# Optimization experiments

Hardware: AMD Instinct MI355X
Metric: run time of the kernel (lower is better)

## Reference

```python
import jax, jax.numpy as jnp
import numpy as np

NUM_EXPERTS = 8
TOP_K = 2
D_HIDDEN = 2048
D_EXPERT = 1024
N_TOKENS = 4096


def setup_inputs() -> dict:
    key = jax.random.key(0)
    ks = jax.random.split(key, 8)
    s_d = 1.0 / np.sqrt(D_HIDDEN).astype(np.float32)
    s_h = 1.0 / np.sqrt(D_EXPERT).astype(np.float32)
    return {
        "x": jax.random.normal(ks[0], (N_TOKENS, D_HIDDEN), jnp.float32),
        "W_g": jax.random.normal(ks[1], (D_HIDDEN, NUM_EXPERTS), jnp.float32) * s_d,
        "W_gate": jax.random.normal(ks[2], (NUM_EXPERTS, D_HIDDEN, D_EXPERT), jnp.float32) * s_d,
        "W_up": jax.random.normal(ks[3], (NUM_EXPERTS, D_HIDDEN, D_EXPERT), jnp.float32) * s_d,
        "W_down": jax.random.normal(ks[4], (NUM_EXPERTS, D_EXPERT, D_HIDDEN), jnp.float32) * s_h,
        "Ws_gate": jax.random.normal(ks[5], (D_HIDDEN, D_EXPERT), jnp.float32) * s_d,
        "Ws_up": jax.random.normal(ks[6], (D_HIDDEN, D_EXPERT), jnp.float32) * s_d,
        "Ws_down": jax.random.normal(ks[7], (D_EXPERT, D_HIDDEN), jnp.float32) * s_h,
    }


def reference(x, W_g, W_gate, W_up, W_down, Ws_gate, Ws_up, Ws_down):
    # Router: softmax logits -> top-k scores/indices (fused_gating_topk)
    probs = jax.nn.softmax(x @ W_g, axis=-1)                      # [N, E]
    scores, idx = jax.lax.top_k(probs, TOP_K)                     # [N, K]
    # Per-(token, expert) combine weight; zero for unrouted experts.
    combine = (jax.nn.one_hot(idx, NUM_EXPERTS, dtype=x.dtype) * scores[..., None]).sum(axis=1)  # [N, E]

    # Routed experts: fused gate/up SiLU with per-token weight scaling, then down-proj.
    gate = jnp.einsum('nd,edh->enh', x, W_gate)                   # [E, N, H]
    up = jnp.einsum('nd,edh->enh', x, W_up)                       # [E, N, H]
    h = jax.nn.silu(gate) * up * combine.T[:, :, None]            # weight=0 kills unrouted tokens
    out = jnp.einsum('enh,ehd->nd', h, W_down)                    # [N, D]

    # Shared expert applied to every token (no routing weight).
    shared = (jax.nn.silu(x @ Ws_gate) * (x @ Ws_up)) @ Ws_down
    return out + shared
```

## Files before the change

kernel.cpp:

```cpp
#include <hip/hip_runtime.h>
#include <cstdint>
#include <cstddef>

#define N_TOK 4096
#define D_HID 2048
#define D_EXP 1024
#define NE 8
#define N_ROUTED (N_TOK * 2)
#define N_ROWS (N_ROUTED + N_TOK)
#define MAX_BLK 56
#define NT1 (D_HID / 32)
#define NT2 (D_EXP / 32)

typedef unsigned short u16;
typedef __bf16 bf16x8 __attribute__((ext_vector_type(8)));
typedef float f32x4 __attribute__((ext_vector_type(4)));

constexpr size_t OFF_XB    = 0;
constexpr size_t OFF_WG    = OFF_XB    + 16777216;
constexpr size_t OFF_WU    = OFF_WG    + 33554432;
constexpr size_t OFF_WD    = OFF_WU    + 33554432;
constexpr size_t OFF_WSG   = OFF_WD    + 33554432;
constexpr size_t OFF_WSU   = OFF_WSG   + 4194304;
constexpr size_t OFF_WSD   = OFF_WSU   + 4194304;
constexpr size_t OFF_H     = OFF_WSD   + 4194304;
constexpr size_t OFF_ROWS  = OFF_H     + 25165824;
constexpr size_t OFF_WSLOT = OFF_ROWS  + 49152;
constexpr size_t OFF_SEG   = OFF_WSLOT + 49152;
constexpr size_t OFF_BLK   = OFF_SEG   + 128;
constexpr size_t OFF_TOPI  = OFF_BLK   + 768;
constexpr size_t OFF_TOPW  = OFF_TOPI  + 32768;
constexpr size_t OFF_INV   = OFF_TOPW  + 32768;
constexpr size_t OFF_H2    = OFF_WG;

__device__ __forceinline__ u16 f32_to_bf16(float f) {
    union { float f; unsigned int u; } c; c.f = f;
    unsigned int u = c.u;
    return (u16)((u + 0x7FFFu + ((u >> 16) & 1u)) >> 16);
}
__device__ __forceinline__ float bf16_to_f32(u16 v) {
    union { unsigned int u; float f; } c; c.u = ((unsigned int)v) << 16;
    return c.f;
}

__device__ __forceinline__ void gld_lds16(const u16* g, u16* l) {
    __builtin_amdgcn_global_load_lds(
        (const __attribute__((address_space(1))) void*)g,
        (__attribute__((address_space(3))) void*)l,
        16, 0, 0);
}

__global__ void cvt_x_kernel(const float* __restrict__ x, u16* __restrict__ xb) {
    size_t i = ((size_t)blockIdx.x * 256 + threadIdx.x) * 8;
    float4 a = *(const float4*)(x + i);
    float4 b = *(const float4*)(x + i + 4);
    union { u16 us[8]; uint4 v; } r;
    r.us[0] = f32_to_bf16(a.x); r.us[1] = f32_to_bf16(a.y);
    r.us[2] = f32_to_bf16(a.z); r.us[3] = f32_to_bf16(a.w);
    r.us[4] = f32_to_bf16(b.x); r.us[5] = f32_to_bf16(b.y);
    r.us[6] = f32_to_bf16(b.z); r.us[7] = f32_to_bf16(b.w);
    *(uint4*)(xb + i) = r.v;
}

__global__ void prep_gu_kernel(const float* __restrict__ Wg, const float* __restrict__ Wu,
                               const float* __restrict__ Wsg, const float* __restrict__ Wsu,
                               u16* __restrict__ Wg_t, u16* __restrict__ Wu_t,
                               u16* __restrict__ Wsg_t, u16* __restrict__ Wsu_t) {
    __shared__ float tile[64][66];
    const int z = blockIdx.z;
    const float* src; u16* dst;
    if (z < 8)        { src = Wg + (size_t)z * (D_HID * D_EXP);       dst = Wg_t + (size_t)z * (D_HID * D_EXP); }
    else if (z < 16)  { src = Wu + (size_t)(z - 8) * (D_HID * D_EXP); dst = Wu_t + (size_t)(z - 8) * (D_HID * D_EXP); }
    else if (z == 16) { src = Wsg; dst = Wsg_t; }
    else              { src = Wsu; dst = Wsu_t; }
    const int c0 = blockIdx.x * 64, r0 = blockIdx.y * 64;
    const int tid = threadIdx.x;
    const int tx = tid & 15, ty = tid >> 4;
#pragma unroll
    for (int i = 0; i < 4; i++) {
        float4 v = *(const float4*)(src + (size_t)(r0 + ty + 16 * i) * D_EXP + c0 + tx * 4);
        tile[ty + 16 * i][tx * 4 + 0] = v.x;
        tile[ty + 16 * i][tx * 4 + 1] = v.y;
        tile[ty + 16 * i][tx * 4 + 2] = v.z;
        tile[ty + 16 * i][tx * 4 + 3] = v.w;
    }
    __syncthreads();
    const int kx = tid & 7, cy = tid >> 3;
#pragma unroll
    for (int j = 0; j < 2; j++) {
        int n = cy + 32 * j;
        union { u16 us[8]; uint4 v; } r;
#pragma unroll
        for (int m = 0; m < 8; m++) r.us[m] = f32_to_bf16(tile[kx * 8 + m][n]);
        *(uint4*)(dst + (size_t)(c0 + n) * D_HID + r0 + kx * 8) = r.v;
    }
}

__global__ void prep_d_kernel(const float* __restrict__ Wd, const float* __restrict__ Wsd,
                              u16* __restrict__ Wd_t, u16* __restrict__ Wsd_t) {
    __shared__ float tile[64][66];
    const int z = blockIdx.z;
    const float* src; u16* dst;
    if (z < 8) { src = Wd + (size_t)z * (D_EXP * D_HID); dst = Wd_t + (size_t)z * (D_EXP * D_HID); }
    else       { src = Wsd; dst = Wsd_t; }
    const int c0 = blockIdx.x * 64, r0 = blockIdx.y * 64;
    const int tid = threadIdx.x;
    const int tx = tid & 15, ty = tid >> 4;
#pragma unroll
    for (int i = 0; i < 4; i++) {
        float4 v = *(const float4*)(src + (size_t)(r0 + ty + 16 * i) * D_HID + c0 + tx * 4);
        tile[ty + 16 * i][tx * 4 + 0] = v.x;
        tile[ty + 16 * i][tx * 4 + 1] = v.y;
        tile[ty + 16 * i][tx * 4 + 2] = v.z;
        tile[ty + 16 * i][tx * 4 + 3] = v.w;
    }
    __syncthreads();
    const int kx = tid & 7, cy = tid >> 3;
#pragma unroll
    for (int j = 0; j < 2; j++) {
        int n = cy + 32 * j;
        union { u16 us[8]; uint4 v; } r;
#pragma unroll
        for (int m = 0; m < 8; m++) r.us[m] = f32_to_bf16(tile[kx * 8 + m][n]);
        *(uint4*)(dst + (size_t)(c0 + n) * D_EXP + r0 + kx * 8) = r.v;
    }
}

__global__ void router_kernel(const float* __restrict__ x, const float* __restrict__ Wg,
                              int* __restrict__ topi, float* __restrict__ topw) {
    const int wave = threadIdx.x >> 6, lane = threadIdx.x & 63;
    const int t = blockIdx.x * 4 + wave;
    const float* xr = x + (size_t)t * D_HID;
    float acc[8] = {0.f, 0.f, 0.f, 0.f, 0.f, 0.f, 0.f, 0.f};
    for (int k = lane; k < D_HID; k += 64) {
        float xv = xr[k];
        float4 w0 = *(const float4*)(Wg + k * 8);
        float4 w1 = *(const float4*)(Wg + k * 8 + 4);
        acc[0] += xv * w0.x; acc[1] += xv * w0.y; acc[2] += xv * w0.z; acc[3] += xv * w0.w;
        acc[4] += xv * w1.x; acc[5] += xv * w1.y; acc[6] += xv * w1.z; acc[7] += xv * w1.w;
    }
#pragma unroll
    for (int e = 0; e < 8; e++)
#pragma unroll
        for (int off = 32; off > 0; off >>= 1)
            acc[e] += __shfl_xor(acc[e], off);
    if (lane == 0) {
        float mx = acc[0];
#pragma unroll
        for (int e = 1; e < 8; e++) mx = fmaxf(mx, acc[e]);
        float p[8], sum = 0.f;
#pragma unroll
        for (int e = 0; e < 8; e++) { p[e] = __expf(acc[e] - mx); sum += p[e]; }
        int i0 = 0; float b0 = p[0];
#pragma unroll
        for (int e = 1; e < 8; e++) if (p[e] > b0) { b0 = p[e]; i0 = e; }
        int i1 = -1; float b1 = -1.f;
#pragma unroll
        for (int e = 0; e < 8; e++) if (e != i0 && p[e] > b1) { b1 = p[e]; i1 = e; }
        float inv = 1.f / sum;
        topi[t * 2] = i0;  topi[t * 2 + 1] = i1;
        topw[t * 2] = b0 * inv; topw[t * 2 + 1] = b1 * inv;
    }
}

__global__ void builder_kernel(const int* __restrict__ topi, const float* __restrict__ topw,
                               int* __restrict__ rows, float* __restrict__ wslot,
                               int* __restrict__ seg, int* __restrict__ blkmap,
                               int* __restrict__ inv) {
    __shared__ int cnt[8], offs[8];
    const int tid = threadIdx.x;
    if (tid < 8) cnt[tid] = 0;
    __syncthreads();
    for (int i = tid; i < N_TOK * 2; i += 256) atomicAdd(&cnt[topi[i]], 1);
    __syncthreads();
    if (tid == 0) {
        int run = 0;
        for (int e = 0; e < 8; e++) {
            offs[e] = run; seg[e] = run; seg[16 + e] = cnt[e]; run += cnt[e];
        }
        seg[8] = N_ROUTED; seg[16 + 8] = N_TOK;
        int nb = 0;
        for (int e = 0; e < 9; e++) {
            int L = (e < 8) ? cnt[e] : N_TOK;
            for (int rb = 0; rb * 256 < L; rb++) blkmap[nb++] = (e << 8) | rb;
        }
        seg[10] = nb;
    }
    __syncthreads();
    for (int i = tid; i < N_TOK * 2; i += 256) {
        int e = topi[i];
        int p = atomicAdd(&offs[e], 1);
        rows[p] = i >> 1;
        wslot[p] = topw[i];
        inv[i] = p;
    }
    for (int t = tid; t < N_TOK; t += 256) {
        rows[N_ROUTED + t] = t;
        wslot[N_ROUTED + t] = 1.0f;
    }
}

__global__ __launch_bounds__(512, 2)
void gemm1_kernel(const u16* __restrict__ xb,
                  const u16* __restrict__ Wg_t, const u16* __restrict__ Wu_t,
                  const u16* __restrict__ Wsg_t, const u16* __restrict__ Wsu_t,
                  const int* __restrict__ rows, const float* __restrict__ wslot,
                  const int* __restrict__ seg, const int* __restrict__ blkmap,
                  u16* __restrict__ h) {
    __shared__ u16 lds[4][16384];
    __shared__ int tok_s[256];
    const int f = blockIdx.x;
    const int iy = f & 7, ix = f >> 3;
    if (ix >= seg[10]) return;
    const int code = blkmap[ix];
    const int e = code >> 8, rb = code & 255;
    const int s = seg[e], L = seg[e + 16];
    const u16* Bg = (e < NE) ? Wg_t + (size_t)e * D_EXP * D_HID : Wsg_t;
    const u16* Bu = (e < NE) ? Wu_t + (size_t)e * D_EXP * D_HID : Wsu_t;
    const int cbase = iy * 128;
    const int tid = threadIdx.x;
    if (tid < 256) {
        int lr = rb * 256 + tid;
        tok_s[tid] = rows[s + (lr < L ? lr : 0)];
    }
    __syncthreads();

    const int l = tid & 63, w = tid >> 6;
    const int rl = l >> 2;
    const int cg = (l & 3) ^ ((l >> 3) & 3);
    const int rowS = w * 16 + rl;
    const u16* gA0 = xb + (size_t)tok_s[rowS] * D_HID + cg * 8;
    const u16* gA1 = xb + (size_t)tok_s[128 + rowS] * D_HID + cg * 8;
    const u16* gBg = Bg + (size_t)(cbase + rowS) * D_HID + cg * 8;
    const u16* gBu = Bu + (size_t)(cbase + rowS) * D_HID + cg * 8;
    const int wbase = w * 512;

    const int wm = w & 1, wn = w >> 1;
    const int ln = l & 15, quad = l >> 4;
    const int pch = (quad ^ ((ln >> 1) & 3)) * 8;
    const int aoff = (wm * 128 + ln) * 32 + pch;
    const int goff = 8192 + (wn * 32 + ln) * 32 + pch;

    f32x4 accg[8][2], accu[8][2];
    const f32x4 zero = {0.f, 0.f, 0.f, 0.f};
#pragma unroll
    for (int i = 0; i < 8; i++)
#pragma unroll
        for (int j = 0; j < 2; j++) { accg[i][j] = zero; accu[i][j] = zero; }

#define STAGE_A1(t) { u16* dst = &lds[(t) & 3][wbase]; \
        gld_lds16(gA0 + (t) * 32, dst); \
        gld_lds16(gA1 + (t) * 32, dst + 4096); }
#define STAGE_B1(t) { u16* dst = &lds[(t) & 3][8192 + wbase]; \
        gld_lds16(gBg + (t) * 32, dst); \
        gld_lds16(gBu + (t) * 32, dst + 4096); }

    STAGE_A1(0); STAGE_B1(0);
    STAGE_A1(1); STAGE_B1(1);
    STAGE_A1(2); STAGE_B1(2);

#pragma unroll 1
    for (int t = 0; t < NT1; ++t) {
        if (t < NT1 - 2)       asm volatile("s_waitcnt vmcnt(8)" ::: "memory");
        else if (t == NT1 - 2) asm volatile("s_waitcnt vmcnt(4)" ::: "memory");
        else                   asm volatile("s_waitcnt vmcnt(0)" ::: "memory");
        __builtin_amdgcn_s_barrier();
        __builtin_amdgcn_sched_barrier(0);
        const u16* bufp = &lds[t & 3][0];
        bf16x8 af[4], bg[2], bu[2];
#pragma unroll
        for (int m = 0; m < 4; m++) af[m] = *(const bf16x8*)(bufp + aoff + m * 512);
#pragma unroll
        for (int n = 0; n < 2; n++) {
            bg[n] = *(const bf16x8*)(bufp + goff + n * 512);
            bu[n] = *(const bf16x8*)(bufp + goff + 4096 + n * 512);
        }
        if (t + 3 < NT1) STAGE_A1(t + 3);
        __builtin_amdgcn_s_barrier();
        asm volatile("s_waitcnt lgkmcnt(0)" ::: "memory");
        __builtin_amdgcn_sched_barrier(0);
        __builtin_amdgcn_s_setprio(1);
#pragma unroll
        for (int n = 0; n < 2; n++)
#pragma unroll
            for (int m = 0; m < 4; m++) {
                accg[m][n] = __builtin_amdgcn_mfma_f32_16x16x32_bf16(af[m], bg[n], accg[m][n], 0, 0, 0);
                accu[m][n] = __builtin_amdgcn_mfma_f32_16x16x32_bf16(af[m], bu[n], accu[m][n], 0, 0, 0);
            }
        __builtin_amdgcn_s_setprio(0);
#pragma unroll
        for (int m = 0; m < 4; m++) af[m] = *(const bf16x8*)(bufp + aoff + (4 + m) * 512);
        if (t + 3 < NT1) STAGE_B1(t + 3);
        __builtin_amdgcn_s_barrier();
        asm volatile("s_waitcnt lgkmcnt(0)" ::: "memory");
        __builtin_amdgcn_sched_barrier(0);
        __builtin_amdgcn_s_setprio(1);
#pragma unroll
        for (int n = 0; n < 2; n++)
#pragma unroll
            for (int m = 0; m < 4; m++) {
                accg[4 + m][n] = __builtin_amdgcn_mfma_f32_16x16x32_bf16(af[m], bg[n], accg[4 + m][n], 0, 0, 0);
                accu[4 + m][n] = __builtin_amdgcn_mfma_f32_16x16x32_bf16(af[m], bu[n], accu[4 + m][n], 0, 0, 0);
            }
        __builtin_amdgcn_s_setprio(0);
    }
#undef STAGE_A1
#undef STAGE_B1

#pragma unroll
    for (int m = 0; m < 8; m++) {
#pragma unroll
        for (int r = 0; r < 4; r++) {
            int lrow = rb * 256 + wm * 128 + m * 16 + quad * 4 + r;
            if (lrow >= L) continue;
            int pos = s + lrow;
            float wgt = wslot[pos];
#pragma unroll
            for (int n = 0; n < 2; n++) {
                float g = accg[m][n][r];
                float u = accu[m][n][r];
                float hv = (g / (1.f + __expf(-g))) * u * wgt;
                h[(size_t)pos * D_EXP + cbase + wn * 32 + n * 16 + ln] = f32_to_bf16(hv);
            }
        }
    }
}

__global__ __launch_bounds__(512, 2)
void gemm2_kernel(const u16* __restrict__ h,
                  const u16* __restrict__ Wd_t, const u16* __restrict__ Wsd_t,
                  const int* __restrict__ seg, const int* __restrict__ blkmap,
                  u16* __restrict__ h2) {
    __shared__ u16 lds[4][16384];
    const int f = blockIdx.x;
    const int iy = f & 7, ix = f >> 3;
    if (ix >= seg[10]) return;
    const int code = blkmap[ix];
    const int e = code >> 8, rb = code & 255;
    const int s = seg[e], L = seg[e + 16];
    const u16* B = (e < NE) ? Wd_t + (size_t)e * D_HID * D_EXP : Wsd_t;
    const int cbase = iy * 256;
    const int tid = threadIdx.x;

    const int l = tid & 63, w = tid >> 6;
    const int rl = l >> 2;
    const int cg = (l & 3) ^ ((l >> 3) & 3);
    const int rowS = w * 16 + rl;
    const u16* gA0 = h + (size_t)(s + rb * 256 + rowS) * D_EXP + cg * 8;
    const u16* gA1 = gA0 + (size_t)128 * D_EXP;
    const u16* gB0 = B + (size_t)(cbase + rowS) * D_EXP + cg * 8;
    const u16* gB1 = gB0 + (size_t)128 * D_EXP;
    const int wbase = w * 512;

    const int wm = w & 1, wn = w >> 1;
    const int ln = l & 15, quad = l >> 4;
    const int pch = (quad ^ ((ln >> 1) & 3)) * 8;
    const int aoff = (wm * 128 + ln) * 32 + pch;
    const int boff = 8192 + (wn * 64 + ln) * 32 + pch;

    f32x4 acc[8][4];
    const f32x4 zero = {0.f, 0.f, 0.f, 0.f};
#pragma unroll
    for (int i = 0; i < 8; i++)
#pragma unroll
        for (int j = 0; j < 4; j++) acc[i][j] = zero;

#define STAGE_A2(t) { u16* dst = &lds[(t) & 3][wbase]; \
        gld_lds16(gA0 + (t) * 32, dst); \
        gld_lds16(gA1 + (t) * 32, dst + 4096); }
#define STAGE_B2(t) { u16* dst = &lds[(t) & 3][8192 + wbase]; \
        gld_lds16(gB0 + (t) * 32, dst); \
        gld_lds16(gB1 + (t) * 32, dst + 4096); }

    STAGE_A2(0); STAGE_B2(0);
    STAGE_A2(1); STAGE_B2(1);
    STAGE_A2(2); STAGE_B2(2);

#pragma unroll 1
    for (int t = 0; t < NT2; ++t) {
        if (t < NT2 - 2)       asm volatile("s_waitcnt vmcnt(8)" ::: "memory");
        else if (t == NT2 - 2) asm volatile("s_waitcnt vmcnt(4)" ::: "memory");
        else                   asm volatile("s_waitcnt vmcnt(0)" ::: "memory");
        __builtin_amdgcn_s_barrier();
        __builtin_amdgcn_sched_barrier(0);
        const u16* bufp = &lds[t & 3][0];
        bf16x8 af[4], bf[4];
#pragma unroll
        for (int m = 0; m < 4; m++) af[m] = *(const bf16x8*)(bufp + aoff + m * 512);
#pragma unroll
        for (int n = 0; n < 4; n++) bf[n] = *(const bf16x8*)(bufp + boff + n * 512);
        if (t + 3 < NT2) STAGE_A2(t + 3);
        __builtin_amdgcn_s_barrier();
        asm volatile("s_waitcnt lgkmcnt(0)" ::: "memory");
        __builtin_amdgcn_sched_barrier(0);
        __builtin_amdgcn_s_setprio(1);
#pragma unroll
        for (int n = 0; n < 4; n++)
#pragma unroll
            for (int m = 0; m < 4; m++)
                acc[m][n] = __builtin_amdgcn_mfma_f32_16x16x32_bf16(af[m], bf[n], acc[m][n], 0, 0, 0);
        __builtin_amdgcn_s_setprio(0);
#pragma unroll
        for (int m = 0; m < 4; m++) af[m] = *(const bf16x8*)(bufp + aoff + (4 + m) * 512);
        if (t + 3 < NT2) STAGE_B2(t + 3);
        __builtin_amdgcn_s_barrier();
        asm volatile("s_waitcnt lgkmcnt(0)" ::: "memory");
        __builtin_amdgcn_sched_barrier(0);
        __builtin_amdgcn_s_setprio(1);
#pragma unroll
        for (int n = 0; n < 4; n++)
#pragma unroll
            for (int m = 0; m < 4; m++)
                acc[4 + m][n] = __builtin_amdgcn_mfma_f32_16x16x32_bf16(af[m], bf[n], acc[4 + m][n], 0, 0, 0);
        __builtin_amdgcn_s_setprio(0);
    }
#undef STAGE_A2
#undef STAGE_B2

#pragma unroll
    for (int m = 0; m < 8; m++) {
#pragma unroll
        for (int r = 0; r < 4; r++) {
            int lrow = rb * 256 + wm * 128 + m * 16 + quad * 4 + r;
            if (lrow >= L) continue;
            size_t slot = (size_t)(s + lrow);
#pragma unroll
            for (int n = 0; n < 4; n++) {
                h2[slot * D_HID + cbase + wn * 64 + n * 16 + ln] = f32_to_bf16(acc[m][n][r]);
            }
        }
    }
}

__global__ void combine_kernel(const u16* __restrict__ h2, const int* __restrict__ inv,
                               float* __restrict__ out) {
    const int t = blockIdx.x;
    const int d = threadIdx.x * 8;
    const size_t r0 = (size_t)inv[t * 2] * D_HID + d;
    const size_t r1 = (size_t)inv[t * 2 + 1] * D_HID + d;
    const size_t r2 = (size_t)(N_ROUTED + t) * D_HID + d;
    union { uint4 v; u16 us[8]; } a, b, c;
    a.v = *(const uint4*)(h2 + r0);
    b.v = *(const uint4*)(h2 + r1);
    c.v = *(const uint4*)(h2 + r2);
    float4 lo, hi;
    lo.x = bf16_to_f32(a.us[0]) + bf16_to_f32(b.us[0]) + bf16_to_f32(c.us[0]);
    lo.y = bf16_to_f32(a.us[1]) + bf16_to_f32(b.us[1]) + bf16_to_f32(c.us[1]);
    lo.z = bf16_to_f32(a.us[2]) + bf16_to_f32(b.us[2]) + bf16_to_f32(c.us[2]);
    lo.w = bf16_to_f32(a.us[3]) + bf16_to_f32(b.us[3]) + bf16_to_f32(c.us[3]);
    hi.x = bf16_to_f32(a.us[4]) + bf16_to_f32(b.us[4]) + bf16_to_f32(c.us[4]);
    hi.y = bf16_to_f32(a.us[5]) + bf16_to_f32(b.us[5]) + bf16_to_f32(c.us[5]);
    hi.z = bf16_to_f32(a.us[6]) + bf16_to_f32(b.us[6]) + bf16_to_f32(c.us[6]);
    hi.w = bf16_to_f32(a.us[7]) + bf16_to_f32(b.us[7]) + bf16_to_f32(c.us[7]);
    float* o = out + (size_t)t * D_HID + d;
    *(float4*)o = lo;
    *(float4*)(o + 4) = hi;
}

extern "C" void kernel_launch(void* const* d_in, const int* in_sizes, int n_in,
                              void* d_out, int out_size, void* d_ws, size_t ws_size,
                              hipStream_t stream) {
    const float* x       = (const float*)d_in[0];
    const float* W_g     = (const float*)d_in[1];
    const float* W_gate  = (const float*)d_in[2];
    const float* W_up    = (const float*)d_in[3];
    const float* W_down  = (const float*)d_in[4];
    const float* Ws_gate = (const float*)d_in[5];
    const float* Ws_up   = (const float*)d_in[6];
    const float* Ws_down = (const float*)d_in[7];
    float* out = (float*)d_out;
    char* ws = (char*)d_ws;

    u16*   xb    = (u16*)(ws + OFF_XB);
    u16*   Wg_t  = (u16*)(ws + OFF_WG);
    u16*   Wu_t  = (u16*)(ws + OFF_WU);
    u16*   Wd_t  = (u16*)(ws + OFF_WD);
    u16*   Wsg_t = (u16*)(ws + OFF_WSG);
    u16*   Wsu_t = (u16*)(ws + OFF_WSU);
    u16*   Wsd_t = (u16*)(ws + OFF_WSD);
    u16*   h     = (u16*)(ws + OFF_H);
    u16*   h2    = (u16*)(ws + OFF_H2);
    int*   rows  = (int*)(ws + OFF_ROWS);
    float* wslot = (float*)(ws + OFF_WSLOT);
    int*   seg   = (int*)(ws + OFF_SEG);
    int*   blkmap= (int*)(ws + OFF_BLK);
    int*   topi  = (int*)(ws + OFF_TOPI);
    float* topw  = (float*)(ws + OFF_TOPW);
    int*   inv   = (int*)(ws + OFF_INV);

    cvt_x_kernel<<<dim3((N_TOK * D_HID) / (256 * 8)), dim3(256), 0, stream>>>(x, xb);
    prep_gu_kernel<<<dim3(D_EXP / 64, D_HID / 64, 18), dim3(256), 0, stream>>>(
        W_gate, W_up, Ws_gate, Ws_up, Wg_t, Wu_t, Wsg_t, Wsu_t);
    prep_d_kernel<<<dim3(D_HID / 64, D_EXP / 64, 9), dim3(256), 0, stream>>>(
        W_down, Ws_down, Wd_t, Wsd_t);

    router_kernel<<<dim3(N_TOK / 4), dim3(256), 0, stream>>>(x, W_g, topi, topw);
    builder_kernel<<<dim3(1), dim3(256), 0, stream>>>(topi, topw, rows, wslot, seg, blkmap, inv);

    gemm1_kernel<<<dim3(MAX_BLK * (D_EXP / 128)), dim3(512), 0, stream>>>(
        xb, Wg_t, Wu_t, Wsg_t, Wsu_t, rows, wslot, seg, blkmap, h);
    gemm2_kernel<<<dim3(MAX_BLK * (D_HID / 256)), dim3(512), 0, stream>>>(
        h, Wd_t, Wsd_t, seg, blkmap, h2);
    combine_kernel<<<dim3(N_TOK), dim3(256), 0, stream>>>(h2, inv, out);
}
```

Baseline: 527.7 us.

## Halve GEMM row tiles to 128, use 256-thread blocks and triple buffering

Both expert GEMM kernels move from 256-row tiles with 512 threads and a 4-deep LDS ring to 128-row tiles with 256 threads and a 3-deep ring prefetching two steps ahead. The router block map is rebuilt at 128-row granularity and MAX_BLK is doubled. Smaller M tiles reduce wasted work on the ragged tail of each expert segment and create more blocks to fill the CUs. In exchange, each B tile is loaded by twice as many blocks, which lowers reuse and raises memory traffic, and the shallower prefetch leaves less latency hiding.

After: 516.4 us. 1.02x faster.

```diff
diff --git a/kernel.cpp b/kernel.cpp
--- a/kernel.cpp
+++ b/kernel.cpp
@@ -8,7 +8,7 @@
 #define NE 8
 #define N_ROUTED (N_TOK * 2)
 #define N_ROWS (N_ROUTED + N_TOK)
-#define MAX_BLK 56
+#define MAX_BLK 112
 #define NT1 (D_HID / 32)
 #define NT2 (D_EXP / 32)
 
@@ -182,7 +182,7 @@
         int nb = 0;
         for (int e = 0; e < 9; e++) {
             int L = (e < 8) ? cnt[e] : N_TOK;
-            for (int rb = 0; rb * 256 < L; rb++) blkmap[nb++] = (e << 8) | rb;
+            for (int rb = 0; rb * 128 < L; rb++) blkmap[nb++] = (e << 8) | rb;
         }
         seg[10] = nb;
     }
@@ -200,15 +200,15 @@
     }
 }
 
-__global__ __launch_bounds__(512, 2)
+__global__ __launch_bounds__(256, 2)
 void gemm1_kernel(const u16* __restrict__ xb,
                   const u16* __restrict__ Wg_t, const u16* __restrict__ Wu_t,
                   const u16* __restrict__ Wsg_t, const u16* __restrict__ Wsu_t,
                   const int* __restrict__ rows, const float* __restrict__ wslot,
                   const int* __restrict__ seg, const int* __restrict__ blkmap,
                   u16* __restrict__ h) {
-    __shared__ u16 lds[4][16384];
-    __shared__ int tok_s[256];
+    __shared__ u16 lds[3][12288];
+    __shared__ int tok_s[128];
     const int f = blockIdx.x;
     const int iy = f & 7, ix = f >> 3;
     if (ix >= seg[10]) return;
@@ -219,8 +219,8 @@
     const u16* Bu = (e < NE) ? Wu_t + (size_t)e * D_EXP * D_HID : Wsu_t;
     const int cbase = iy * 128;
     const int tid = threadIdx.x;
-    if (tid < 256) {
-        int lr = rb * 256 + tid;
+    if (tid < 128) {
+        int lr = rb * 128 + tid;
         tok_s[tid] = rows[s + (lr < L ? lr : 0)];
     }
     __syncthreads();
@@ -229,109 +229,117 @@
     const int rl = l >> 2;
     const int cg = (l & 3) ^ ((l >> 3) & 3);
     const int rowS = w * 16 + rl;
-    const u16* gA0 = xb + (size_t)tok_s[rowS] * D_HID + cg * 8;
-    const u16* gA1 = xb + (size_t)tok_s[128 + rowS] * D_HID + cg * 8;
-    const u16* gBg = Bg + (size_t)(cbase + rowS) * D_HID + cg * 8;
-    const u16* gBu = Bu + (size_t)(cbase + rowS) * D_HID + cg * 8;
+    const u16* gA0  = xb + (size_t)tok_s[rowS] * D_HID + cg * 8;
+    const u16* gA1  = xb + (size_t)tok_s[64 + rowS] * D_HID + cg * 8;
+    const u16* gBg0 = Bg + (size_t)(cbase + rowS) * D_HID + cg * 8;
+    const u16* gBg1 = Bg + (size_t)(cbase + 64 + rowS) * D_HID + cg * 8;
+    const u16* gBu0 = Bu + (size_t)(cbase + rowS) * D_HID + cg * 8;
+    const u16* gBu1 = Bu + (size_t)(cbase + 64 + rowS) * D_HID + cg * 8;
     const int wbase = w * 512;
 
     const int wm = w & 1, wn = w >> 1;
     const int ln = l & 15, quad = l >> 4;
     const int pch = (quad ^ ((ln >> 1) & 3)) * 8;
-    const int aoff = (wm * 128 + ln) * 32 + pch;
-    const int goff = 8192 + (wn * 32 + ln) * 32 + pch;
-
-    f32x4 accg[8][2], accu[8][2];
+    const int aoff = (wm * 64 + ln) * 32 + pch;
+    const int goff = 4096 + (wn * 64 + ln) * 32 + pch;
+    const int uoff = 8192 + (wn * 64 + ln) * 32 + pch;
+
+    f32x4 accg[4][4], accu[4][4];
     const f32x4 zero = {0.f, 0.f, 0.f, 0.f};
 #pragma unroll
-    for (int i = 0; i < 8; i++)
-#pragma unroll
-        for (int j = 0; j < 2; j++) { accg[i][j] = zero; accu[i][j] = zero; }
-
-#define STAGE_A1(t) { u16* dst = &lds[(t) & 3][wbase]; \
-        gld_lds16(gA0 + (t) * 32, dst); \
-        gld_lds16(gA1 + (t) * 32, dst + 4096); }
-#define STAGE_B1(t) { u16* dst = &lds[(t) & 3][8192 + wbase]; \
-        gld_lds16(gBg + (t) * 32, dst); \
-        gld_lds16(gBu + (t) * 32, dst + 4096); }
-
-    STAGE_A1(0); STAGE_B1(0);
-    STAGE_A1(1); STAGE_B1(1);
-    STAGE_A1(2); STAGE_B1(2);
-
+    for (int i = 0; i < 4; i++)
+#pragma unroll
+        for (int j = 0; j < 4; j++) { accg[i][j] = zero; accu[i][j] = zero; }
+
+#define STAGE_A1(t, d) { \
+        gld_lds16(gA0 + (t) * 32, (d) + wbase); \
+        gld_lds16(gA1 + (t) * 32, (d) + 2048 + wbase); }
+#define STAGE_B1(t, d) { \
+        gld_lds16(gBg0 + (t) * 32, (d) + 4096 + wbase); \
+        gld_lds16(gBg1 + (t) * 32, (d) + 6144 + wbase); \
+        gld_lds16(gBu0 + (t) * 32, (d) + 8192 + wbase); \
+        gld_lds16(gBu1 + (t) * 32, (d) + 10240 + wbase); }
+
+    STAGE_A1(0, &lds[0][0]); STAGE_B1(0, &lds[0][0]);
+    STAGE_A1(1, &lds[1][0]); STAGE_B1(1, &lds[1][0]);
+
+    int cur = 0;
 #pragma unroll 1
     for (int t = 0; t < NT1; ++t) {
-        if (t < NT1 - 2)       asm volatile("s_waitcnt vmcnt(8)" ::: "memory");
-        else if (t == NT1 - 2) asm volatile("s_waitcnt vmcnt(4)" ::: "memory");
-        else                   asm volatile("s_waitcnt vmcnt(0)" ::: "memory");
+        if (t < NT1 - 1) asm volatile("s_waitcnt vmcnt(6)" ::: "memory");
+        else             asm volatile("s_waitcnt vmcnt(0)" ::: "memory");
         __builtin_amdgcn_s_barrier();
         __builtin_amdgcn_sched_barrier(0);
-        const u16* bufp = &lds[t & 3][0];
-        bf16x8 af[4], bg[2], bu[2];
-#pragma unroll
-        for (int m = 0; m < 4; m++) af[m] = *(const bf16x8*)(bufp + aoff + m * 512);
-#pragma unroll
-        for (int n = 0; n < 2; n++) {
+        const u16* bufp = &lds[cur][0];
+        int stb = cur + 2; if (stb >= 3) stb -= 3;
+        u16* sdst = &lds[stb][0];
+        const bool do_stage = (t + 2 < NT1);
+        bf16x8 af[2], bg[4], bu[4];
+#pragma unroll
+        for (int m = 0; m < 2; m++) af[m] = *(const bf16x8*)(bufp + aoff + m * 512);
+#pragma unroll
+        for (int n = 0; n < 4; n++) {
             bg[n] = *(const bf16x8*)(bufp + goff + n * 512);
-            bu[n] = *(const bf16x8*)(bufp + goff + 4096 + n * 512);
+            bu[n] = *(const bf16x8*)(bufp + uoff + n * 512);
         }
-        if (t + 3 < NT1) STAGE_A1(t + 3);
+        if (do_stage) STAGE_A1(t + 2, sdst);
         __builtin_amdgcn_s_barrier();
         asm volatile("s_waitcnt lgkmcnt(0)" ::: "memory");
         __builtin_amdgcn_sched_barrier(0);
         __builtin_amdgcn_s_setprio(1);
 #pragma unroll
-        for (int n = 0; n < 2; n++)
-#pragma unroll
-            for (int m = 0; m < 4; m++) {
+        for (int n = 0; n < 4; n++)
+#pragma unroll
+            for (int m = 0; m < 2; m++) {
                 accg[m][n] = __builtin_amdgcn_mfma_f32_16x16x32_bf16(af[m], bg[n], accg[m][n], 0, 0, 0);
                 accu[m][n] = __builtin_amdgcn_mfma_f32_16x16x32_bf16(af[m], bu[n], accu[m][n], 0, 0, 0);
             }
         __builtin_amdgcn_s_setprio(0);
 #pragma unroll
-        for (int m = 0; m < 4; m++) af[m] = *(const bf16x8*)(bufp + aoff + (4 + m) * 512);
-        if (t + 3 < NT1) STAGE_B1(t + 3);
+        for (int m = 0; m < 2; m++) af[m] = *(const bf16x8*)(bufp + aoff + (2 + m) * 512);
+        if (do_stage) STAGE_B1(t + 2, sdst);
         __builtin_amdgcn_s_barrier();
         asm volatile("s_waitcnt lgkmcnt(0)" ::: "memory");
         __builtin_amdgcn_sched_barrier(0);
         __builtin_amdgcn_s_setprio(1);
 #pragma unroll
-        for (int n = 0; n < 2; n++)
-#pragma unroll
-            for (int m = 0; m < 4; m++) {
-                accg[4 + m][n] = __builtin_amdgcn_mfma_f32_16x16x32_bf16(af[m], bg[n], accg[4 + m][n], 0, 0, 0);
-                accu[4 + m][n] = __builtin_amdgcn_mfma_f32_16x16x32_bf16(af[m], bu[n], accu[4 + m][n], 0, 0, 0);
+        for (int n = 0; n < 4; n++)
+#pragma unroll
+            for (int m = 0; m < 2; m++) {
+                accg[2 + m][n] = __builtin_amdgcn_mfma_f32_16x16x32_bf16(af[m], bg[n], accg[2 + m][n], 0, 0, 0);
+                accu[2 + m][n] = __builtin_amdgcn_mfma_f32_16x16x32_bf16(af[m], bu[n], accu[2 + m][n], 0, 0, 0);
             }
         __builtin_amdgcn_s_setprio(0);
+        cur++; if (cur >= 3) cur = 0;
     }
 #undef STAGE_A1
 #undef STAGE_B1
 
 #pragma unroll
-    for (int m = 0; m < 8; m++) {
+    for (int m = 0; m < 4; m++) {
 #pragma unroll
         for (int r = 0; r < 4; r++) {
-            int lrow = rb * 256 + wm * 128 + m * 16 + quad * 4 + r;
+            int lrow = rb * 128 + wm * 64 + m * 16 + quad * 4 + r;
             if (lrow >= L) continue;
             int pos = s + lrow;
             float wgt = wslot[pos];
 #pragma unroll
-            for (int n = 0; n < 2; n++) {
+            for (int n = 0; n < 4; n++) {
                 float g = accg[m][n][r];
                 float u = accu[m][n][r];
                 float hv = (g / (1.f + __expf(-g))) * u * wgt;
-                h[(size_t)pos * D_EXP + cbase + wn * 32 + n * 16 + ln] = f32_to_bf16(hv);
+                h[(size_t)pos * D_EXP + cbase + wn * 64 + n * 16 + ln] = f32_to_bf16(hv);
             }
         }
     }
 }
 
-__global__ __launch_bounds__(512, 2)
+__global__ __launch_bounds__(256, 2)
 void gemm2_kernel(const u16* __restrict__ h,
                   const u16* __restrict__ Wd_t, const u16* __restrict__ Wsd_t,
                   const int* __restrict__ seg, const int* __restrict__ blkmap,
                   u16* __restrict__ h2) {
-    __shared__ u16 lds[4][16384];
+    __shared__ u16 lds[3][12288];
     const int f = blockIdx.x;
     const int iy = f & 7, ix = f >> 3;
     if (ix >= seg[10]) return;
@@ -346,87 +354,94 @@
     const int rl = l >> 2;
     const int cg = (l & 3) ^ ((l >> 3) & 3);
     const int rowS = w * 16 + rl;
-    const u16* gA0 = h + (size_t)(s + rb * 256 + rowS) * D_EXP + cg * 8;
-    const u16* gA1 = gA0 + (size_t)128 * D_EXP;
+    const u16* gA0 = h + (size_t)(s + rb * 128 + rowS) * D_EXP + cg * 8;
+    const u16* gA1 = gA0 + (size_t)64 * D_EXP;
     const u16* gB0 = B + (size_t)(cbase + rowS) * D_EXP + cg * 8;
-    const u16* gB1 = gB0 + (size_t)128 * D_EXP;
+    const u16* gB1 = gB0 + (size_t)64 * D_EXP;
+    const u16* gB2 = gB0 + (size_t)128 * D_EXP;
+    const u16* gB3 = gB0 + (size_t)192 * D_EXP;
     const int wbase = w * 512;
 
     const int wm = w & 1, wn = w >> 1;
     const int ln = l & 15, quad = l >> 4;
     const int pch = (quad ^ ((ln >> 1) & 3)) * 8;
-    const int aoff = (wm * 128 + ln) * 32 + pch;
-    const int boff = 8192 + (wn * 64 + ln) * 32 + pch;
-
-    f32x4 acc[8][4];
+    const int aoff = (wm * 64 + ln) * 32 + pch;
+    const int boff = 4096 + (wn * 128 + ln) * 32 + pch;
+
+    f32x4 acc[4][8];
     const f32x4 zero = {0.f, 0.f, 0.f, 0.f};
 #pragma unroll
-    for (int i = 0; i < 8; i++)
-#pragma unroll
-        for (int j = 0; j < 4; j++) acc[i][j] = zero;
-
-#define STAGE_A2(t) { u16* dst = &lds[(t) & 3][wbase]; \
-        gld_lds16(gA0 + (t) * 32, dst); \
-        gld_lds16(gA1 + (t) * 32, dst + 4096); }
-#define STAGE_B2(t) { u16* dst = &lds[(t) & 3][8192 + wbase]; \
-        gld_lds16(gB0 + (t) * 32, dst); \
-        gld_lds16(gB1 + (t) * 32, dst + 4096); }
-
-    STAGE_A2(0); STAGE_B2(0);
-    STAGE_A2(1); STAGE_B2(1);
-    STAGE_A2(2); STAGE_B2(2);
-
+    for (int i = 0; i < 4; i++)
+#pragma unroll
+        for (int j = 0; j < 8; j++) acc[i][j] = zero;
+
+#define STAGE_A2(t, d) { \
+        gld_lds16(gA0 + (t) * 32, (d) + wbase); \
+        gld_lds16(gA1 + (t) * 32, (d) + 2048 + wbase); }
+#define STAGE_B2(t, d) { \
+        gld_lds16(gB0 + (t) * 32, (d) + 4096 + wbase); \
+        gld_lds16(gB1 + (t) * 32, (d) + 6144 + wbase); \
+        gld_lds16(gB2 + (t) * 32, (d) + 8192 + wbase); \
+        gld_lds16(gB3 + (t) * 32, (d) + 10240 + wbase); }
+
+    STAGE_A2(0, &lds[0][0]); STAGE_B2(0, &lds[0][0]);
+    STAGE_A2(1, &lds[1][0]); STAGE_B2(1, &lds[1][0]);
+
+    int cur = 0;
 #pragma unroll 1
     for (int t = 0; t < NT2; ++t) {
-        if (t < NT2 - 2)       asm volatile("s_waitcnt vmcnt(8)" ::: "memory");
-        else if (t == NT2 - 2) asm volatile("s_waitcnt vmcnt(4)" ::: "memory");
-        else                   asm volatile("s_waitcnt vmcnt(0)" ::: "memory");
+        if (t < NT2 - 1) asm volatile("s_waitcnt vmcnt(6)" ::: "memory");
+        else             asm volatile("s_waitcnt vmcnt(0)" ::: "memory");
         __builtin_amdgcn_s_barrier();
         __builtin_amdgcn_sched_barrier(0);
-        const u16* bufp = &lds[t & 3][0];
-        bf16x8 af[4], bf[4];
-#pragma unroll
-        for (int m = 0; m < 4; m++) af[m] = *(const bf16x8*)(bufp + aoff + m * 512);
-#pragma unroll
-        for (int n = 0; n < 4; n++) bf[n] = *(const bf16x8*)(bufp + boff + n * 512);
-        if (t + 3 < NT2) STAGE_A2(t + 3);
+        const u16* bufp = &lds[cur][0];
+        int stb = cur + 2; if (stb >= 3) stb -= 3;
+        u16* sdst = &lds[stb][0];
+        const bool do_stage = (t + 2 < NT2);
+        bf16x8 af[2], bf[8];
+#pragma unroll
+        for (int m = 0; m < 2; m++) af[m] = *(const bf16x8*)(bufp + aoff + m * 512);
+#pragma unroll
+        for (int n = 0; n < 8; n++) bf[n] = *(const bf16x8*)(bufp + boff + n * 512);
+        if (do_stage) STAGE_A2(t + 2, sdst);
         __builtin_amdgcn_s_barrier();
         asm volatile("s_waitcnt lgkmcnt(0)" ::: "memory");
         __builtin_amdgcn_sched_barrier(0);
         __builtin_amdgcn_s_setprio(1);
 #pragma unroll
-        for (int n = 0; n < 4; n++)
-#pragma unroll
-            for (int m = 0; m < 4; m++)
+        for (int n = 0; n < 8; n++)
+#pragma unroll
+            for (int m = 0; m < 2; m++)
                 acc[m][n] = __builtin_amdgcn_mfma_f32_16x16x32_bf16(af[m], bf[n], acc[m][n], 0, 0, 0);
         __builtin_amdgcn_s_setprio(0);
 #pragma unroll
-        for (int m = 0; m < 4; m++) af[m] = *(const bf16x8*)(bufp + aoff + (4 + m) * 512);
-        if (t + 3 < NT2) STAGE_B2(t + 3);
+        for (int m = 0; m < 2; m++) af[m] = *(const bf16x8*)(bufp + aoff + (2 + m) * 512);
+        if (do_stage) STAGE_B2(t + 2, sdst);
         __builtin_amdgcn_s_barrier();
         asm volatile("s_waitcnt lgkmcnt(0)" ::: "memory");
         __builtin_amdgcn_sched_barrier(0);
         __builtin_amdgcn_s_setprio(1);
 #pragma unroll
-        for (int n = 0; n < 4; n++)
-#pragma unroll
-            for (int m = 0; m < 4; m++)
-                acc[4 + m][n] = __builtin_amdgcn_mfma_f32_16x16x32_bf16(af[m], bf[n], acc[4 + m][n], 0, 0, 0);
+        for (int n = 0; n < 8; n++)
+#pragma unroll
+            for (int m = 0; m < 2; m++)
+                acc[2 + m][n] = __builtin_amdgcn_mfma_f32_16x16x32_bf16(af[m], bf[n], acc[2 + m][n], 0, 0, 0);
         __builtin_amdgcn_s_setprio(0);
+        cur++; if (cur >= 3) cur = 0;
     }
 #undef STAGE_A2
 #undef STAGE_B2
 
 #pragma unroll
-    for (int m = 0; m < 8; m++) {
+    for (int m = 0; m < 4; m++) {
 #pragma unroll
         for (int r = 0; r < 4; r++) {
-            int lrow = rb * 256 + wm * 128 + m * 16 + quad * 4 + r;
+            int lrow = rb * 128 + wm * 64 + m * 16 + quad * 4 + r;
             if (lrow >= L) continue;
             size_t slot = (size_t)(s + lrow);
 #pragma unroll
-            for (int n = 0; n < 4; n++) {
-                h2[slot * D_HID + cbase + wn * 64 + n * 16 + ln] = f32_to_bf16(acc[m][n][r]);
+            for (int n = 0; n < 8; n++) {
+                h2[slot * D_HID + cbase + wn * 128 + n * 16 + ln] = f32_to_bf16(acc[m][n][r]);
             }
         }
     }
@@ -497,9 +512,9 @@
     router_kernel<<<dim3(N_TOK / 4), dim3(256), 0, stream>>>(x, W_g, topi, topw);
     builder_kernel<<<dim3(1), dim3(256), 0, stream>>>(topi, topw, rows, wslot, seg, blkmap, inv);
 
-    gemm1_kernel<<<dim3(MAX_BLK * (D_EXP / 128)), dim3(512), 0, stream>>>(
+    gemm1_kernel<<<dim3(MAX_BLK * 8), dim3(256), 0, stream>>>(
         xb, Wg_t, Wu_t, Wsg_t, Wsu_t, rows, wslot, seg, blkmap, h);
-    gemm2_kernel<<<dim3(MAX_BLK * (D_HID / 256)), dim3(512), 0, stream>>>(
+    gemm2_kernel<<<dim3(MAX_BLK * 8), dim3(256), 0, stream>>>(
         h, Wd_t, Wsd_t, seg, blkmap, h2);
     combine_kernel<<<dim3(N_TOK), dim3(256), 0, stream>>>(h2, inv, out);
 }
```
